# Kernel tuning notes

Measured on AMD Instinct MI355X. Metric: run time of the kernel, lower is better.

## Reference

```python
import jax, jax.numpy as jnp
import numpy as np

N = 50000
E = 300000
NEG_SLOPE = 0.2
EPS = 1e-16


def setup_inputs() -> dict:
    key = jax.random.key(0)
    ks = jax.random.split(key, 12)
    x = jax.random.normal(ks[0], (N, 27), dtype=jnp.float32)
    edge_index = jax.random.randint(ks[1], (2, E), 0, N, dtype=jnp.int64)
    # layer 1: in=27 -> heads1=4, dim=64
    W1 = jax.random.normal(ks[2], (27, 4 * 64), dtype=jnp.float32) * 0.1
    a_src1 = jax.random.normal(ks[3], (4, 64), dtype=jnp.float32) * 0.1
    a_dst1 = jax.random.normal(ks[4], (4, 64), dtype=jnp.float32) * 0.1
    b1 = jnp.zeros((4 * 64,), dtype=jnp.float32)
    # layer 2: in=256 -> heads2=2, dim=64
    W2 = jax.random.normal(ks[5], (256, 2 * 64), dtype=jnp.float32) * 0.05
    a_src2 = jax.random.normal(ks[6], (2, 64), dtype=jnp.float32) * 0.1
    a_dst2 = jax.random.normal(ks[7], (2, 64), dtype=jnp.float32) * 0.1
    b2 = jnp.zeros((2 * 64,), dtype=jnp.float32)
    # final linear: 128 -> 1
    Wfc = jax.random.normal(ks[8], (128, 1), dtype=jnp.float32) * 0.05
    bfc = jnp.zeros((1,), dtype=jnp.float32)
    return {"x": x, "edge_index": edge_index, "W1": W1, "a_src1": a_src1,
            "a_dst1": a_dst1, "b1": b1, "W2": W2, "a_src2": a_src2,
            "a_dst2": a_dst2, "b2": b2, "Wfc": Wfc, "bfc": bfc}


def gat_layer(x, src, dst, W, a_src, a_dst, b, heads, dim):
    # h: [N, H, D]
    h = (x @ W).reshape(N, heads, dim)
    # per-node attention half-scores: [N, H]
    s_src = jnp.einsum('nhd,hd->nh', h, a_src)
    s_dst = jnp.einsum('nhd,hd->nh', h, a_dst)
    # per-edge logits (gather) + leaky relu: [E', H]
    logits = jax.nn.leaky_relu(s_src[src] + s_dst[dst], negative_slope=NEG_SLOPE)
    # segment softmax over incoming edges at each destination node
    m = jax.ops.segment_max(logits, dst, num_segments=N)  # [N, H]
    m = jnp.where(jnp.isfinite(m), m, 0.0)
    e = jnp.exp(logits - m[dst])
    z = jax.ops.segment_sum(e, dst, num_segments=N)  # [N, H]
    alpha = e / (z[dst] + EPS)
    # weighted scatter-aggregate of source features
    out = jax.ops.segment_sum(h[src] * alpha[:, :, None], dst, num_segments=N)
    return out.reshape(N, heads * dim) + b


def reference(x, edge_index, W1, a_src1, a_dst1, b1, W2, a_src2, a_dst2, b2, Wfc, bfc):
    # add self-loops (PyG GATConv default add_self_loops=True)
    loops = jnp.arange(N, dtype=edge_index.dtype)
    src = jnp.concatenate([edge_index[0], loops])
    dst = jnp.concatenate([edge_index[1], loops])
    h = gat_layer(x, src, dst, W1, a_src1, a_dst1, b1, heads=4, dim=64)
    h = jax.nn.elu(h)
    h = gat_layer(h, src, dst, W2, a_src2, a_dst2, b2, heads=2, dim=64)
    h = jax.nn.elu(h)
    out = h @ Wfc + bfc
    return jax.nn.sigmoid(out)
```

## Files before the change

### kernel.cpp

```cpp
#include <hip/hip_runtime.h>
#include <math.h>

#define N_NODES 50000
#define N_PAD   50016
#define E_EDGES 300000
#define E_TOT   350000
#define NEG 0.2f
#define EPS 1e-16f
#define CAP 32
#define PLANE (N_PAD * 32)

typedef __attribute__((ext_vector_type(8))) short bf16x8;
typedef __attribute__((ext_vector_type(4))) float f32x4;

__device__ __forceinline__ float leaky(float x) { return x > 0.f ? x : NEG * x; }
__device__ __forceinline__ short f2bf(float v) {
    unsigned u = __float_as_uint(v);
    u += 0x7fffu + ((u >> 16) & 1u);
    return (short)(u >> 16);
}
__device__ __forceinline__ float bflo(unsigned u) { return __uint_as_float(u << 16); }
__device__ __forceinline__ float bfhi(unsigned u) { return __uint_as_float(u & 0xffff0000u); }
__device__ __forceinline__ unsigned bfpack(short a, short b) {
    return (unsigned)(unsigned short)a | ((unsigned)(unsigned short)b << 16);
}

__global__ __launch_bounds__(256) void k_scatter_s1(const int* __restrict__ ei,
        int* __restrict__ cnt, int* __restrict__ eidx,
        const float* __restrict__ x,
        const float* __restrict__ W1, const float* __restrict__ as1,
        const float* __restrict__ ad1, const float* __restrict__ W2,
        float* __restrict__ s1, short* __restrict__ xb,
        short* __restrict__ W1b, short* __restrict__ W2bT) {
    __shared__ float wsvL[216];
    int t = blockIdx.x * 256 + threadIdx.x;
    if (threadIdx.x < 216) {
        int k = threadIdx.x >> 3, j = threadIdx.x & 7;
        const float* av = (j < 4) ? (as1 + j * 64) : (ad1 + (j - 4) * 64);
        const float* wr = W1 + k * 256 + ((j & 3) * 64);
        float s = 0.f;
        #pragma unroll
        for (int d = 0; d < 64; ++d) s += wr[d] * av[d];
        wsvL[threadIdx.x] = s;
    }
    if (t < E_TOT) {
        int s = (t < E_EDGES) ? ei[t] : (t - E_EDGES);
        int d = (t < E_EDGES) ? ei[E_EDGES + t] : (t - E_EDGES);
        int pos = atomicAdd(&cnt[d], 1);
        if (pos < CAP) eidx[d * CAP + pos] = s;
    }
    if (t < 32768) {
        int col = t >> 8, k = t & 255;
        W2bT[t] = f2bf(W2[k * 128 + col]);
    }
    if (t < 8192) {
        int h = t >> 11, col = (t >> 5) & 63, k = t & 31;
        W1b[t] = f2bf(k < 27 ? W1[k * 256 + h * 64 + col] : 0.f);
    }
    __syncthreads();
    if (t < N_NODES * 8) {
        int n = t >> 3, j = t & 7;
        float s = 0.f;
        #pragma unroll
        for (int k = 0; k < 27; ++k) s += x[n * 27 + k] * wsvL[k * 8 + j];
        s1[t] = s;
        int c0 = j * 4;
        short p0 = f2bf(c0 + 0 < 27 ? x[n * 27 + c0 + 0] : 0.f);
        short p1 = f2bf(c0 + 1 < 27 ? x[n * 27 + c0 + 1] : 0.f);
        short p2 = f2bf(c0 + 2 < 27 ? x[n * 27 + c0 + 2] : 0.f);
        short p3 = f2bf(c0 + 3 < 27 ? x[n * 27 + c0 + 3] : 0.f);
        uint2 wv;
        wv.x = bfpack(p0, p1);
        wv.y = bfpack(p2, p3);
        *(uint2*)(xb + n * 32 + c0) = wv;
    }
}

__global__ __launch_bounds__(256) void k_gather1(const int* __restrict__ cnt,
        const int* __restrict__ eidx, const short* __restrict__ xb,
        const float* __restrict__ s1, short* __restrict__ xagg) {
    int g = threadIdx.x >> 4;
    int q = threadIdx.x & 15;
    int n = blockIdx.x * 16 + g;
    int c2 = 2 * q;
    if (n >= N_NODES) {
        if (n < N_PAD) {
            *(unsigned*)(xagg + 0 * PLANE + n * 32 + c2) = 0u;
            *(unsigned*)(xagg + 1 * PLANE + n * 32 + c2) = 0u;
            *(unsigned*)(xagg + 2 * PLANE + n * 32 + c2) = 0u;
            *(unsigned*)(xagg + 3 * PLANE + n * 32 + c2) = 0u;
        }
        return;
    }
    int beg = n * CAP;
    int espec = eidx[beg + q];
    int deg = min(cnt[n], CAP);
    int myi = (q < deg) ? espec : n;
    float4 sdv = *(const float4*)(s1 + n * 8 + 4);
    float a0 = 0.f, a1 = 0.f, a2 = 0.f, a3 = 0.f;
    float b0 = 0.f, b1v = 0.f, b2v = 0.f, b3 = 0.f;
    float z0 = 0.f, z1 = 0.f, z2 = 0.f, z3 = 0.f;
    float4 svq = *(const float4*)(s1 + myi * 8);
    float me0 = __expf(leaky(svq.x + sdv.x));
    float me1 = __expf(leaky(svq.y + sdv.y));
    float me2 = __expf(leaky(svq.z + sdv.z));
    float me3 = __expf(leaky(svq.w + sdv.w));
    int degw = deg;
    degw = max(degw, __shfl_xor(degw, 16));
    degw = max(degw, __shfl_xor(degw, 32));
    if (degw <= 16) {
        int lw = deg - 1;
        for (int i = 0; i < degw; i += 4) {
            bool m0 = i < deg, m1 = (i + 1) < deg;
            bool m2 = (i + 2) < deg, m3 = (i + 3) < deg;
            int j0 = m0 ? i : lw;
            int j1 = m1 ? i + 1 : lw;
            int j2 = m2 ? i + 2 : lw;
            int j3 = m3 ? i + 3 : lw;
            float g0 = m0 ? 1.f : 0.f, g1 = m1 ? 1.f : 0.f;
            float g2 = m2 ? 1.f : 0.f, g3 = m3 ? 1.f : 0.f;
            int s0 = __shfl(myi, j0, 16);
            int s1i = __shfl(myi, j1, 16);
            int s2i = __shfl(myi, j2, 16);
            int s3 = __shfl(myi, j3, 16);
            float e00 = g0 * __shfl(me0, j0, 16);
            float e01 = g0 * __shfl(me1, j0, 16);
            float e02 = g0 * __shfl(me2, j0, 16);
            float e03 = g0 * __shfl(me3, j0, 16);
            float e10 = g1 * __shfl(me0, j1, 16);
            float e11 = g1 * __shfl(me1, j1, 16);
            float e12 = g1 * __shfl(me2, j1, 16);
            float e13 = g1 * __shfl(me3, j1, 16);
            float e20 = g2 * __shfl(me0, j2, 16);
            float e21 = g2 * __shfl(me1, j2, 16);
            float e22 = g2 * __shfl(me2, j2, 16);
            float e23 = g2 * __shfl(me3, j2, 16);
            float e30 = g3 * __shfl(me0, j3, 16);
            float e31 = g3 * __shfl(me1, j3, 16);
            float e32 = g3 * __shfl(me2, j3, 16);
            float e33 = g3 * __shfl(me3, j3, 16);
            unsigned xv0 = *(const unsigned*)(xb + s0 * 32 + 2 * q);
            unsigned xv1 = *(const unsigned*)(xb + s1i * 32 + 2 * q);
            unsigned xv2 = *(const unsigned*)(xb + s2i * 32 + 2 * q);
            unsigned xv3 = *(const unsigned*)(xb + s3 * 32 + 2 * q);
            float xa0 = bflo(xv0), xc0 = bfhi(xv0);
            float xa1 = bflo(xv1), xc1 = bfhi(xv1);
            float xa2 = bflo(xv2), xc2 = bfhi(xv2);
            float xa3 = bflo(xv3), xc3 = bfhi(xv3);
            z0 += e00 + e10 + e20 + e30;
            z1 += e01 + e11 + e21 + e31;
            z2 += e02 + e12 + e22 + e32;
            z3 += e03 + e13 + e23 + e33;
            a0 += e00 * xa0 + e10 * xa1 + e20 * xa2 + e30 * xa3;
            a1 += e01 * xa0 + e11 * xa1 + e21 * xa2 + e31 * xa3;
            a2 += e02 * xa0 + e12 * xa1 + e22 * xa2 + e32 * xa3;
            a3 += e03 * xa0 + e13 * xa1 + e23 * xa2 + e33 * xa3;
            b0  += e00 * xc0 + e10 * xc1 + e20 * xc2 + e30 * xc3;
            b1v += e01 * xc0 + e11 * xc1 + e21 * xc2 + e31 * xc3;
            b2v += e02 * xc0 + e12 * xc1 + e22 * xc2 + e32 * xc3;
            b3  += e03 * xc0 + e13 * xc1 + e23 * xc2 + e33 * xc3;
        }
    } else {
        int last = beg + deg - 1;
        for (int i = 0; i < deg; i += 4) {
            bool m1 = (i + 1) < deg, m2 = (i + 2) < deg, m3 = (i + 3) < deg;
            int p0 = beg + i;
            int p1 = m1 ? p0 + 1 : last;
            int p2 = m2 ? p0 + 2 : last;
            int p3 = m3 ? p0 + 3 : last;
            int s0 = eidx[p0];
            int s1i = eidx[p1];
            int s2i = eidx[p2];
            int s3 = eidx[p3];
            float4 sv0 = *(const float4*)(s1 + s0 * 8);
            float4 sv1 = *(const float4*)(s1 + s1i * 8);
            float4 sv2 = *(const float4*)(s1 + s2i * 8);
            float4 sv3 = *(const float4*)(s1 + s3 * 8);
            unsigned xv0 = *(const unsigned*)(xb + s0 * 32 + 2 * q);
            unsigned xv1 = *(const unsigned*)(xb + s1i * 32 + 2 * q);
            unsigned xv2 = *(const unsigned*)(xb + s2i * 32 + 2 * q);
            unsigned xv3 = *(const unsigned*)(xb + s3 * 32 + 2 * q);
            float xa0 = bflo(xv0), xc0 = bfhi(xv0);
            float xa1 = bflo(xv1), xc1 = bfhi(xv1);
            float xa2 = bflo(xv2), xc2 = bfhi(xv2);
            float xa3 = bflo(xv3), xc3 = bfhi(xv3);
            float g1 = m1 ? 1.f : 0.f, g2 = m2 ? 1.f : 0.f, g3 = m3 ? 1.f : 0.f;
            float e00 = __expf(leaky(sv0.x + sdv.x));
            float e01 = __expf(leaky(sv0.y + sdv.y));
            float e02 = __expf(leaky(sv0.z + sdv.z));
            float e03 = __expf(leaky(sv0.w + sdv.w));
            float e10 = g1 * __expf(leaky(sv1.x + sdv.x));
            float e11 = g1 * __expf(leaky(sv1.y + sdv.y));
            float e12 = g1 * __expf(leaky(sv1.z + sdv.z));
            float e13 = g1 * __expf(leaky(sv1.w + sdv.w));
            float e20 = g2 * __expf(leaky(sv2.x + sdv.x));
            float e21 = g2 * __expf(leaky(sv2.y + sdv.y));
            float e22 = g2 * __expf(leaky(sv2.z + sdv.z));
            float e23 = g2 * __expf(leaky(sv2.w + sdv.w));
            float e30 = g3 * __expf(leaky(sv3.x + sdv.x));
            float e31 = g3 * __expf(leaky(sv3.y + sdv.y));
            float e32 = g3 * __expf(leaky(sv3.z + sdv.z));
            float e33 = g3 * __expf(leaky(sv3.w + sdv.w));
            z0 += e00 + e10 + e20 + e30;
            z1 += e01 + e11 + e21 + e31;
            z2 += e02 + e12 + e22 + e32;
            z3 += e03 + e13 + e23 + e33;
            a0 += e00 * xa0 + e10 * xa1 + e20 * xa2 + e30 * xa3;
            a1 += e01 * xa0 + e11 * xa1 + e21 * xa2 + e31 * xa3;
            a2 += e02 * xa0 + e12 * xa1 + e22 * xa2 + e32 * xa3;
            a3 += e03 * xa0 + e13 * xa1 + e23 * xa2 + e33 * xa3;
            b0  += e00 * xc0 + e10 * xc1 + e20 * xc2 + e30 * xc3;
            b1v += e01 * xc0 + e11 * xc1 + e21 * xc2 + e31 * xc3;
            b2v += e02 * xc0 + e12 * xc1 + e22 * xc2 + e32 * xc3;
            b3  += e03 * xc0 + e13 * xc1 + e23 * xc2 + e33 * xc3;
        }
    }
    float i0 = 1.f / (z0 + EPS), i1 = 1.f / (z1 + EPS);
    float i2 = 1.f / (z2 + EPS), i3 = 1.f / (z3 + EPS);
    *(unsigned*)(xagg + 0 * PLANE + n * 32 + c2) = bfpack(f2bf(a0 * i0), f2bf(b0 * i0));
    *(unsigned*)(xagg + 1 * PLANE + n * 32 + c2) = bfpack(f2bf(a1 * i1), f2bf(b1v * i1));
    *(unsigned*)(xagg + 2 * PLANE + n * 32 + c2) = bfpack(f2bf(a2 * i2), f2bf(b2v * i2));
    *(unsigned*)(xagg + 3 * PLANE + n * 32 + c2) = bfpack(f2bf(a3 * i3), f2bf(b3 * i3));
}

__global__ __launch_bounds__(256) void k_dense(const short* __restrict__ xagg,
        const short* __restrict__ W1b, const short* __restrict__ W2bT,
        const float* __restrict__ b1, const float* __restrict__ as2,
        const float* __restrict__ ad2, short* __restrict__ h2b,
        float* __restrict__ s2) {
    __shared__ short O[32 * 264];
    __shared__ float P[4][2][32];
    int w = threadIdx.x >> 6, l = threadIdx.x & 63;
    int lane16 = l & 15, quad = l >> 4;
    int n0 = blockIdx.x * 32;
    f32x4 z4 = {0.f, 0.f, 0.f, 0.f};

    {
        bf16x8 am0 = *(const bf16x8*)&xagg[w * PLANE + (n0 + lane16) * 32 + quad * 8];
        bf16x8 am1 = *(const bf16x8*)&xagg[w * PLANE + (n0 + 16 + lane16) * 32 + quad * 8];
        f32x4 c0[4], c1[4];
        #pragma unroll
        for (int nt = 0; nt < 4; ++nt) {
            bf16x8 b = *(const bf16x8*)&W1b[w * 2048 + (nt * 16 + lane16) * 32 + quad * 8];
            c0[nt] = __builtin_amdgcn_mfma_f32_16x16x32_bf16(am0, b, z4, 0, 0, 0);
            c1[nt] = __builtin_amdgcn_mfma_f32_16x16x32_bf16(am1, b, z4, 0, 0, 0);
        }
        #pragma unroll
        for (int nt = 0; nt < 4; ++nt) {
            int col = w * 64 + nt * 16 + lane16;
            float bb = b1[col];
            #pragma unroll
            for (int r2 = 0; r2 < 4; ++r2) {
                float v = c0[nt][r2] + bb;
                v = v > 0.f ? v : __expf(v) - 1.f;
                O[(quad * 4 + r2) * 264 + col] = f2bf(v);
                float u = c1[nt][r2] + bb;
                u = u > 0.f ? u : __expf(u) - 1.f;
                O[(16 + quad * 4 + r2) * 264 + col] = f2bf(u);
            }
        }
    }
    __syncthreads();

    f32x4 acc[2][2];
    acc[0][0] = z4; acc[0][1] = z4; acc[1][0] = z4; acc[1][1] = z4;
    for (int k0 = 0; k0 < 256; k0 += 32) {
        bf16x8 a0 = *(const bf16x8*)&O[lane16 * 264 + k0 + quad * 8];
        bf16x8 a1 = *(const bf16x8*)&O[(16 + lane16) * 264 + k0 + quad * 8];
        #pragma unroll
        for (int j = 0; j < 2; ++j) {
            int ct = 2 * w + j;
            bf16x8 b2 = *(const bf16x8*)&W2bT[(ct * 16 + lane16) * 256 + k0 + quad * 8];
            acc[0][j] = __builtin_amdgcn_mfma_f32_16x16x32_bf16(a0, b2, acc[0][j], 0, 0, 0);
            acc[1][j] = __builtin_amdgcn_mfma_f32_16x16x32_bf16(a1, b2, acc[1][j], 0, 0, 0);
        }
    }
    float ps[2][4] = {{0.f,0.f,0.f,0.f},{0.f,0.f,0.f,0.f}};
    float pd[2][4] = {{0.f,0.f,0.f,0.f},{0.f,0.f,0.f,0.f}};
    #pragma unroll
    for (int j = 0; j < 2; ++j) {
        int col = (2 * w + j) * 16 + lane16;
        float a_s = as2[col], a_d = ad2[col];
        #pragma unroll
        for (int m = 0; m < 2; ++m) {
            #pragma unroll
            for (int r2 = 0; r2 < 4; ++r2) {
                ps[m][r2] += acc[m][j][r2] * a_s;
                pd[m][r2] += acc[m][j][r2] * a_d;
                int row = n0 + m * 16 + quad * 4 + r2;
                if (row < N_NODES) h2b[row * 128 + col] = f2bf(acc[m][j][r2]);
            }
        }
    }
    #pragma unroll
    for (int off = 1; off <= 8; off <<= 1)
        #pragma unroll
        for (int m = 0; m < 2; ++m)
            #pragma unroll
            for (int r2 = 0; r2 < 4; ++r2) {
                ps[m][r2] += __shfl_xor(ps[m][r2], off);
                pd[m][r2] += __shfl_xor(pd[m][r2], off);
            }
    if (lane16 == 0) {
        #pragma unroll
        for (int m = 0; m < 2; ++m)
            #pragma unroll
            for (int r2 = 0; r2 < 4; ++r2) {
                P[w][0][m * 16 + quad * 4 + r2] = ps[m][r2];
                P[w][1][m * 16 + quad * 4 + r2] = pd[m][r2];
            }
    }
    __syncthreads();
    if (threadIdx.x < 64) {
        int m = threadIdx.x & 31, hd = threadIdx.x >> 5;
        int row = n0 + m;
        if (row < N_NODES) {
            s2[row * 4 + hd]     = P[2 * hd][0][m] + P[2 * hd + 1][0][m];
            s2[row * 4 + 2 + hd] = P[2 * hd][1][m] + P[2 * hd + 1][1][m];
        }
    }
}

__global__ __launch_bounds__(256) void k_agg2_csr(const int* __restrict__ cnt,
        const int* __restrict__ eidx, const float* __restrict__ s2,
        const short* __restrict__ h2b, const float* __restrict__ b2,
        const float* __restrict__ Wfc, const float* __restrict__ bfc,
        float* __restrict__ out) {
    int g = threadIdx.x >> 4;
    int q = threadIdx.x & 15;
    int n = blockIdx.x * 16 + g;
    int beg = n * CAP;
    int espec = eidx[beg + q];
    int deg = min(cnt[n], CAP);
    int myi = (q < deg) ? espec : n;
    int h = q >> 3;
    float2 sdv = *(const float2*)(s2 + n * 4 + 2);
    float4 accA = make_float4(0.f, 0.f, 0.f, 0.f);
    float4 accB = make_float4(0.f, 0.f, 0.f, 0.f);
    float z = 0.f;
    float2 svq = *(const float2*)(s2 + myi * 4);
    float mea = __expf(leaky(svq.x + sdv.x));
    float meb = __expf(leaky(svq.y + sdv.y));
    int degw = deg;
    degw = max(degw, __shfl_xor(degw, 16));
    degw = max(degw, __shfl_xor(degw, 32));
    if (degw <= 16) {
        int lw = deg - 1;
        for (int i = 0; i < degw; i += 4) {
            bool m0 = i < deg, m1 = (i + 1) < deg;
            bool m2 = (i + 2) < deg, m3 = (i + 3) < deg;
            int j0 = m0 ? i : lw;
            int j1 = m1 ? i + 1 : lw;
            int j2 = m2 ? i + 2 : lw;
            int j3 = m3 ? i + 3 : lw;
            int a0 = __shfl(myi, j0, 16);
            int a1 = __shfl(myi, j1, 16);
            int a2 = __shfl(myi, j2, 16);
            int a3 = __shfl(myi, j3, 16);
            float ea0 = __shfl(mea, j0, 16), eb0 = __shfl(meb, j0, 16);
            float ea1 = __shfl(mea, j1, 16), eb1 = __shfl(meb, j1, 16);
            float ea2 = __shfl(mea, j2, 16), eb2 = __shfl(meb, j2, 16);
            float ea3 = __shfl(mea, j3, 16), eb3 = __shfl(meb, j3, 16);
            float e0 = (m0 ? 1.f : 0.f) * (h ? eb0 : ea0);
            float e1 = (m1 ? 1.f : 0.f) * (h ? eb1 : ea1);
            float e2 = (m2 ? 1.f : 0.f) * (h ? eb2 : ea2);
            float e3 = (m3 ? 1.f : 0.f) * (h ? eb3 : ea3);
            uint4 v0 = *(const uint4*)(h2b + a0 * 128 + q * 8);
            uint4 v1 = *(const uint4*)(h2b + a1 * 128 + q * 8);
            uint4 v2 = *(const uint4*)(h2b + a2 * 128 + q * 8);
            uint4 v3 = *(const uint4*)(h2b + a3 * 128 + q * 8);
            z += e0 + e1 + e2 + e3;
            accA.x += e0 * bflo(v0.x) + e1 * bflo(v1.x) + e2 * bflo(v2.x) + e3 * bflo(v3.x);
            accA.y += e0 * bfhi(v0.x) + e1 * bfhi(v1.x) + e2 * bfhi(v2.x) + e3 * bfhi(v3.x);
            accA.z += e0 * bflo(v0.y) + e1 * bflo(v1.y) + e2 * bflo(v2.y) + e3 * bflo(v3.y);
            accA.w += e0 * bfhi(v0.y) + e1 * bfhi(v1.y) + e2 * bfhi(v2.y) + e3 * bfhi(v3.y);
            accB.x += e0 * bflo(v0.z) + e1 * bflo(v1.z) + e2 * bflo(v2.z) + e3 * bflo(v3.z);
            accB.y += e0 * bfhi(v0.z) + e1 * bfhi(v1.z) + e2 * bfhi(v2.z) + e3 * bfhi(v3.z);
            accB.z += e0 * bflo(v0.w) + e1 * bflo(v1.w) + e2 * bflo(v2.w) + e3 * bflo(v3.w);
            accB.w += e0 * bfhi(v0.w) + e1 * bfhi(v1.w) + e2 * bfhi(v2.w) + e3 * bfhi(v3.w);
        }
    } else {
        float sd = h ? sdv.y : sdv.x;
        int i = 0;
        for (; i + 4 <= deg; i += 4) {
            int a0 = eidx[beg + i], a1 = eidx[beg + i + 1];
            int a2 = eidx[beg + i + 2], a3 = eidx[beg + i + 3];
            float e0 = __expf(leaky(s2[a0 * 4 + h] + sd));
            float e1 = __expf(leaky(s2[a1 * 4 + h] + sd));
            float e2 = __expf(leaky(s2[a2 * 4 + h] + sd));
            float e3 = __expf(leaky(s2[a3 * 4 + h] + sd));
            uint4 v0 = *(const uint4*)(h2b + a0 * 128 + q * 8);
            uint4 v1 = *(const uint4*)(h2b + a1 * 128 + q * 8);
            uint4 v2 = *(const uint4*)(h2b + a2 * 128 + q * 8);
            uint4 v3 = *(const uint4*)(h2b + a3 * 128 + q * 8);
            z += e0 + e1 + e2 + e3;
            accA.x += e0 * bflo(v0.x) + e1 * bflo(v1.x) + e2 * bflo(v2.x) + e3 * bflo(v3.x);
            accA.y += e0 * bfhi(v0.x) + e1 * bfhi(v1.x) + e2 * bfhi(v2.x) + e3 * bfhi(v3.x);
            accA.z += e0 * bflo(v0.y) + e1 * bflo(v1.y) + e2 * bflo(v2.y) + e3 * bflo(v3.y);
            accA.w += e0 * bfhi(v0.y) + e1 * bfhi(v1.y) + e2 * bfhi(v2.y) + e3 * bfhi(v3.y);
            accB.x += e0 * bflo(v0.z) + e1 * bflo(v1.z) + e2 * bflo(v2.z) + e3 * bflo(v3.z);
            accB.y += e0 * bfhi(v0.z) + e1 * bfhi(v1.z) + e2 * bfhi(v2.z) + e3 * bfhi(v3.z);
            accB.z += e0 * bflo(v0.w) + e1 * bflo(v1.w) + e2 * bflo(v2.w) + e3 * bflo(v3.w);
            accB.w += e0 * bfhi(v0.w) + e1 * bfhi(v1.w) + e2 * bfhi(v2.w) + e3 * bfhi(v3.w);
        }
        for (; i < deg; ++i) {
            int a0 = eidx[beg + i];
            float e0 = __expf(leaky(s2[a0 * 4 + h] + sd));
            uint4 v0 = *(const uint4*)(h2b + a0 * 128 + q * 8);
            z += e0;
            accA.x += e0 * bflo(v0.x); accA.y += e0 * bfhi(v0.x);
            accA.z += e0 * bflo(v0.y); accA.w += e0 * bfhi(v0.y);
            accB.x += e0 * bflo(v0.z); accB.y += e0 * bfhi(v0.z);
            accB.z += e0 * bflo(v0.w); accB.w += e0 * bfhi(v0.w);
        }
    }
    float inv = 1.f / (z + EPS);
    int c0 = q * 8;
    float p = 0.f;
    float va[8] = {accA.x, accA.y, accA.z, accA.w, accB.x, accB.y, accB.z, accB.w};
    #pragma unroll
    for (int j = 0; j < 8; ++j) {
        float v = va[j] * inv + b2[c0 + j];
        v = v > 0.f ? v : __expf(v) - 1.f;
        p += v * Wfc[c0 + j];
    }
    #pragma unroll
    for (int off = 1; off <= 8; off <<= 1) p += __shfl_xor(p, off);
    if (q == 0) out[n] = 1.f / (1.f + __expf(-(p + bfc[0])));
}

extern "C" void kernel_launch(void* const* d_in, const int* in_sizes, int n_in,
                              void* d_out, int out_size, void* d_ws, size_t ws_size,
                              hipStream_t stream) {
    const float* x   = (const float*)d_in[0];
    const int*   ei  = (const int*)d_in[1];
    const float* W1  = (const float*)d_in[2];
    const float* as1 = (const float*)d_in[3];
    const float* ad1 = (const float*)d_in[4];
    const float* b1  = (const float*)d_in[5];
    const float* W2  = (const float*)d_in[6];
    const float* as2 = (const float*)d_in[7];
    const float* ad2 = (const float*)d_in[8];
    const float* b2  = (const float*)d_in[9];
    const float* Wfc = (const float*)d_in[10];
    const float* bfc = (const float*)d_in[11];
    float* out = (float*)d_out;

    float* f = (float*)d_ws;
    short* h2b   = (short*)f;
    float* s1    = f + 3200000;
    float* s2    = f + 3600000;
    int*   cnt   = (int*)(f + 3810000);
    int*   eidx  = (int*)(f + 3870000);
    short* W1b   = (short*)(f + 5500000);
    short* W2bT  = (short*)(f + 5510000);
    short* xb    = (short*)(f + 5530000);
    short* xagg  = (short*)(f + 6400000);

    hipMemsetAsync(cnt, 0, N_NODES * sizeof(int), stream);

    k_scatter_s1<<<1563, 256, 0, stream>>>(ei, cnt, eidx, x, W1, as1, ad1, W2,
                                           s1, xb, W1b, W2bT);

    k_gather1<<<3126, 256, 0, stream>>>(cnt, eidx, xb, s1, xagg);

    k_dense<<<1563, 256, 0, stream>>>(xagg, W1b, W2bT, b1, as2, ad2, h2b, s2);

    k_agg2_csr<<<3125, 256, 0, stream>>>(cnt, eidx, s2, h2b, b2, Wfc, bfc, out);
}
```

Baseline: 167.7 us.

## Widen layer-2 aggregation to 32 lanes per node, batch gathers, stage x in LDS

The layer-2 aggregation kernel now gives each node 32 lanes with 4 channels each instead of 16 lanes with 8 channels, and the launch grid doubles to match. Both gather kernels replace the 4-wide masked loop with fixed 8-edge batches whose loads are issued together before accumulation, aiming for more memory-level parallelism on the random gathers. The first kernel stages each block's x rows in shared memory so they are read from global memory once rather than repeatedly per thread. The trade-off is padded work for low-degree nodes, since at least 8 slots are always processed, plus the added reduction step and thread count.

```diff
diff --git a/kernel.cpp b/kernel.cpp
--- a/kernel.cpp
+++ b/kernel.cpp
@@ -33,15 +33,23 @@
         float* __restrict__ s1, short* __restrict__ xb,
         short* __restrict__ W1b, short* __restrict__ W2bT) {
     __shared__ float wsvL[216];
-    int t = blockIdx.x * 256 + threadIdx.x;
-    if (threadIdx.x < 216) {
-        int k = threadIdx.x >> 3, j = threadIdx.x & 7;
+    __shared__ float xL[32 * 27];
+    int tid = threadIdx.x;
+    int t = blockIdx.x * 256 + tid;
+    int nb = blockIdx.x * 32;
+    #pragma unroll
+    for (int i = tid; i < 864; i += 256) {
+        int gi = nb * 27 + i;
+        xL[i] = (gi < N_NODES * 27) ? x[gi] : 0.f;
+    }
+    if (tid < 216) {
+        int k = tid >> 3, j = tid & 7;
         const float* av = (j < 4) ? (as1 + j * 64) : (ad1 + (j - 4) * 64);
         const float* wr = W1 + k * 256 + ((j & 3) * 64);
         float s = 0.f;
         #pragma unroll
         for (int d = 0; d < 64; ++d) s += wr[d] * av[d];
-        wsvL[threadIdx.x] = s;
+        wsvL[tid] = s;
     }
     if (t < E_TOT) {
         int s = (t < E_EDGES) ? ei[t] : (t - E_EDGES);
@@ -59,20 +67,22 @@
     }
     __syncthreads();
     if (t < N_NODES * 8) {
-        int n = t >> 3, j = t & 7;
+        int ln = tid >> 3, j = tid & 7;
+        int n = nb + ln;
         float s = 0.f;
         #pragma unroll
-        for (int k = 0; k < 27; ++k) s += x[n * 27 + k] * wsvL[k * 8 + j];
+        for (int k = 0; k < 27; ++k) s += xL[ln * 27 + k] * wsvL[k * 8 + j];
         s1[t] = s;
         int c0 = j * 4;
-        short p0 = f2bf(c0 + 0 < 27 ? x[n * 27 + c0 + 0] : 0.f);
-        short p1 = f2bf(c0 + 1 < 27 ? x[n * 27 + c0 + 1] : 0.f);
-        short p2 = f2bf(c0 + 2 < 27 ? x[n * 27 + c0 + 2] : 0.f);
-        short p3 = f2bf(c0 + 3 < 27 ? x[n * 27 + c0 + 3] : 0.f);
+        short p0 = f2bf(c0 + 0 < 27 ? xL[ln * 27 + c0 + 0] : 0.f);
+        short p1 = f2bf(c0 + 1 < 27 ? xL[ln * 27 + c0 + 1] : 0.f);
+        short p2 = f2bf(c0 + 2 < 27 ? xL[ln * 27 + c0 + 2] : 0.f);
+        short p3 = f2bf(c0 + 3 < 27 ? xL[ln * 27 + c0 + 3] : 0.f);
         uint2 wv;
         wv.x = bfpack(p0, p1);
         wv.y = bfpack(p2, p3);
         *(uint2*)(xb + n * 32 + c0) = wv;
+        (void)n;
     }
 }
 
@@ -109,56 +119,45 @@
     degw = max(degw, __shfl_xor(degw, 16));
     degw = max(degw, __shfl_xor(degw, 32));
     if (degw <= 16) {
-        int lw = deg - 1;
-        for (int i = 0; i < degw; i += 4) {
-            bool m0 = i < deg, m1 = (i + 1) < deg;
-            bool m2 = (i + 2) < deg, m3 = (i + 3) < deg;
-            int j0 = m0 ? i : lw;
-            int j1 = m1 ? i + 1 : lw;
-            int j2 = m2 ? i + 2 : lw;
-            int j3 = m3 ? i + 3 : lw;
-            float g0 = m0 ? 1.f : 0.f, g1 = m1 ? 1.f : 0.f;
-            float g2 = m2 ? 1.f : 0.f, g3 = m3 ? 1.f : 0.f;
-            int s0 = __shfl(myi, j0, 16);
-            int s1i = __shfl(myi, j1, 16);
-            int s2i = __shfl(myi, j2, 16);
-            int s3 = __shfl(myi, j3, 16);
-            float e00 = g0 * __shfl(me0, j0, 16);
-            float e01 = g0 * __shfl(me1, j0, 16);
-            float e02 = g0 * __shfl(me2, j0, 16);
-            float e03 = g0 * __shfl(me3, j0, 16);
-            float e10 = g1 * __shfl(me0, j1, 16);
-            float e11 = g1 * __shfl(me1, j1, 16);
-            float e12 = g1 * __shfl(me2, j1, 16);
-            float e13 = g1 * __shfl(me3, j1, 16);
-            float e20 = g2 * __shfl(me0, j2, 16);
-            float e21 = g2 * __shfl(me1, j2, 16);
-            float e22 = g2 * __shfl(me2, j2, 16);
-            float e23 = g2 * __shfl(me3, j2, 16);
-            float e30 = g3 * __shfl(me0, j3, 16);
-            float e31 = g3 * __shfl(me1, j3, 16);
-            float e32 = g3 * __shfl(me2, j3, 16);
-            float e33 = g3 * __shfl(me3, j3, 16);
-            unsigned xv0 = *(const unsigned*)(xb + s0 * 32 + 2 * q);
-            unsigned xv1 = *(const unsigned*)(xb + s1i * 32 + 2 * q);
-            unsigned xv2 = *(const unsigned*)(xb + s2i * 32 + 2 * q);
-            unsigned xv3 = *(const unsigned*)(xb + s3 * 32 + 2 * q);
-            float xa0 = bflo(xv0), xc0 = bfhi(xv0);
-            float xa1 = bflo(xv1), xc1 = bfhi(xv1);
-            float xa2 = bflo(xv2), xc2 = bfhi(xv2);
-            float xa3 = bflo(xv3), xc3 = bfhi(xv3);
-            z0 += e00 + e10 + e20 + e30;
-            z1 += e01 + e11 + e21 + e31;
-            z2 += e02 + e12 + e22 + e32;
-            z3 += e03 + e13 + e23 + e33;
-            a0 += e00 * xa0 + e10 * xa1 + e20 * xa2 + e30 * xa3;
-            a1 += e01 * xa0 + e11 * xa1 + e21 * xa2 + e31 * xa3;
-            a2 += e02 * xa0 + e12 * xa1 + e22 * xa2 + e32 * xa3;
-            a3 += e03 * xa0 + e13 * xa1 + e23 * xa2 + e33 * xa3;
-            b0  += e00 * xc0 + e10 * xc1 + e20 * xc2 + e30 * xc3;
-            b1v += e01 * xc0 + e11 * xc1 + e21 * xc2 + e31 * xc3;
-            b2v += e02 * xc0 + e12 * xc1 + e22 * xc2 + e32 * xc3;
-            b3  += e03 * xc0 + e13 * xc1 + e23 * xc2 + e33 * xc3;
+        {
+            unsigned xv[8];
+            #pragma unroll
+            for (int j = 0; j < 8; ++j) {
+                int sj = __shfl(myi, j, 16);
+                xv[j] = *(const unsigned*)(xb + sj * 32 + c2);
+            }
+            #pragma unroll
+            for (int j = 0; j < 8; ++j) {
+                float gj = (j < deg) ? 1.f : 0.f;
+                float e0 = gj * __shfl(me0, j, 16);
+                float e1 = gj * __shfl(me1, j, 16);
+                float e2 = gj * __shfl(me2, j, 16);
+                float e3 = gj * __shfl(me3, j, 16);
+                float xa = bflo(xv[j]), xc = bfhi(xv[j]);
+                z0 += e0; z1 += e1; z2 += e2; z3 += e3;
+                a0 += e0 * xa; a1 += e1 * xa; a2 += e2 * xa; a3 += e3 * xa;
+                b0 += e0 * xc; b1v += e1 * xc; b2v += e2 * xc; b3 += e3 * xc;
+            }
+        }
+        if (degw > 8) {
+            unsigned xv[8];
+            #pragma unroll
+            for (int j = 0; j < 8; ++j) {
+                int sj = __shfl(myi, 8 + j, 16);
+                xv[j] = *(const unsigned*)(xb + sj * 32 + c2);
+            }
+            #pragma unroll
+            for (int j = 0; j < 8; ++j) {
+                float gj = (8 + j < deg) ? 1.f : 0.f;
+                float e0 = gj * __shfl(me0, 8 + j, 16);
+                float e1 = gj * __shfl(me1, 8 + j, 16);
+                float e2 = gj * __shfl(me2, 8 + j, 16);
+                float e3 = gj * __shfl(me3, 8 + j, 16);
+                float xa = bflo(xv[j]), xc = bfhi(xv[j]);
+                z0 += e0; z1 += e1; z2 += e2; z3 += e3;
+                a0 += e0 * xa; a1 += e1 * xa; a2 += e2 * xa; a3 += e3 * xa;
+                b0 += e0 * xc; b1v += e1 * xc; b2v += e2 * xc; b3 += e3 * xc;
+            }
         }
     } else {
         int last = beg + deg - 1;
@@ -176,10 +175,10 @@
             float4 sv1 = *(const float4*)(s1 + s1i * 8);
             float4 sv2 = *(const float4*)(s1 + s2i * 8);
             float4 sv3 = *(const float4*)(s1 + s3 * 8);
-            unsigned xv0 = *(const unsigned*)(xb + s0 * 32 + 2 * q);
-            unsigned xv1 = *(const unsigned*)(xb + s1i * 32 + 2 * q);
-            unsigned xv2 = *(const unsigned*)(xb + s2i * 32 + 2 * q);
-            unsigned xv3 = *(const unsigned*)(xb + s3 * 32 + 2 * q);
+            unsigned xv0 = *(const unsigned*)(xb + s0 * 32 + c2);
+            unsigned xv1 = *(const unsigned*)(xb + s1i * 32 + c2);
+            unsigned xv2 = *(const unsigned*)(xb + s2i * 32 + c2);
+            unsigned xv3 = *(const unsigned*)(xb + s3 * 32 + c2);
             float xa0 = bflo(xv0), xc0 = bfhi(xv0);
             float xa1 = bflo(xv1), xc1 = bfhi(xv1);
             float xa2 = bflo(xv2), xc2 = bfhi(xv2);
@@ -326,58 +325,54 @@
         const short* __restrict__ h2b, const float* __restrict__ b2,
         const float* __restrict__ Wfc, const float* __restrict__ bfc,
         float* __restrict__ out) {
-    int g = threadIdx.x >> 4;
-    int q = threadIdx.x & 15;
-    int n = blockIdx.x * 16 + g;
+    int g = threadIdx.x >> 5;
+    int q = threadIdx.x & 31;
+    int n = blockIdx.x * 8 + g;
     int beg = n * CAP;
-    int espec = eidx[beg + q];
+    int q16 = q & 15;
+    int espec = eidx[beg + q16];
     int deg = min(cnt[n], CAP);
-    int myi = (q < deg) ? espec : n;
-    int h = q >> 3;
+    int myi = (q16 < deg) ? espec : n;
+    int h = q >> 4;
     float2 sdv = *(const float2*)(s2 + n * 4 + 2);
-    float4 accA = make_float4(0.f, 0.f, 0.f, 0.f);
-    float4 accB = make_float4(0.f, 0.f, 0.f, 0.f);
+    float ac0 = 0.f, ac1 = 0.f, ac2 = 0.f, ac3 = 0.f;
     float z = 0.f;
     float2 svq = *(const float2*)(s2 + myi * 4);
     float mea = __expf(leaky(svq.x + sdv.x));
     float meb = __expf(leaky(svq.y + sdv.y));
-    int degw = deg;
-    degw = max(degw, __shfl_xor(degw, 16));
-    degw = max(degw, __shfl_xor(degw, 32));
+    int degw = max(deg, __shfl_xor(deg, 32));
     if (degw <= 16) {
-        int lw = deg - 1;
-        for (int i = 0; i < degw; i += 4) {
-            bool m0 = i < deg, m1 = (i + 1) < deg;
-            bool m2 = (i + 2) < deg, m3 = (i + 3) < deg;
-            int j0 = m0 ? i : lw;
-            int j1 = m1 ? i + 1 : lw;
-            int j2 = m2 ? i + 2 : lw;
-            int j3 = m3 ? i + 3 : lw;
-            int a0 = __shfl(myi, j0, 16);
-            int a1 = __shfl(myi, j1, 16);
-            int a2 = __shfl(myi, j2, 16);
-            int a3 = __shfl(myi, j3, 16);
-            float ea0 = __shfl(mea, j0, 16), eb0 = __shfl(meb, j0, 16);
-            float ea1 = __shfl(mea, j1, 16), eb1 = __shfl(meb, j1, 16);
-            float ea2 = __shfl(mea, j2, 16), eb2 = __shfl(meb, j2, 16);
-            float ea3 = __shfl(mea, j3, 16), eb3 = __shfl(meb, j3, 16);
-            float e0 = (m0 ? 1.f : 0.f) * (h ? eb0 : ea0);
-            float e1 = (m1 ? 1.f : 0.f) * (h ? eb1 : ea1);
-            float e2 = (m2 ? 1.f : 0.f) * (h ? eb2 : ea2);
-            float e3 = (m3 ? 1.f : 0.f) * (h ? eb3 : ea3);
-            uint4 v0 = *(const uint4*)(h2b + a0 * 128 + q * 8);
-            uint4 v1 = *(const uint4*)(h2b + a1 * 128 + q * 8);
-            uint4 v2 = *(const uint4*)(h2b + a2 * 128 + q * 8);
-            uint4 v3 = *(const uint4*)(h2b + a3 * 128 + q * 8);
-            z += e0 + e1 + e2 + e3;
-            accA.x += e0 * bflo(v0.x) + e1 * bflo(v1.x) + e2 * bflo(v2.x) + e3 * bflo(v3.x);
-            accA.y += e0 * bfhi(v0.x) + e1 * bfhi(v1.x) + e2 * bfhi(v2.x) + e3 * bfhi(v3.x);
-            accA.z += e0 * bflo(v0.y) + e1 * bflo(v1.y) + e2 * bflo(v2.y) + e3 * bflo(v3.y);
-            accA.w += e0 * bfhi(v0.y) + e1 * bfhi(v1.y) + e2 * bfhi(v2.y) + e3 * bfhi(v3.y);
-            accB.x += e0 * bflo(v0.z) + e1 * bflo(v1.z) + e2 * bflo(v2.z) + e3 * bflo(v3.z);
-            accB.y += e0 * bfhi(v0.z) + e1 * bfhi(v1.z) + e2 * bfhi(v2.z) + e3 * bfhi(v3.z);
-            accB.z += e0 * bflo(v0.w) + e1 * bflo(v1.w) + e2 * bflo(v2.w) + e3 * bflo(v3.w);
-            accB.w += e0 * bfhi(v0.w) + e1 * bfhi(v1.w) + e2 * bfhi(v2.w) + e3 * bfhi(v3.w);
+        {
+            uint2 v[8];
+            #pragma unroll
+            for (int j = 0; j < 8; ++j) {
+                int aj = __shfl(myi, j, 32);
+                v[j] = *(const uint2*)(h2b + aj * 128 + q * 4);
+            }
+            #pragma unroll
+            for (int j = 0; j < 8; ++j) {
+                float ea = __shfl(mea, j, 32), eb = __shfl(meb, j, 32);
+                float e = ((j < deg) ? 1.f : 0.f) * (h ? eb : ea);
+                z += e;
+                ac0 += e * bflo(v[j].x); ac1 += e * bfhi(v[j].x);
+                ac2 += e * bflo(v[j].y); ac3 += e * bfhi(v[j].y);
+            }
+        }
+        if (degw > 8) {
+            uint2 v[8];
+            #pragma unroll
+            for (int j = 0; j < 8; ++j) {
+                int aj = __shfl(myi, 8 + j, 32);
+                v[j] = *(const uint2*)(h2b + aj * 128 + q * 4);
+            }
+            #pragma unroll
+            for (int j = 0; j < 8; ++j) {
+                float ea = __shfl(mea, 8 + j, 32), eb = __shfl(meb, 8 + j, 32);
+                float e = ((8 + j < deg) ? 1.f : 0.f) * (h ? eb : ea);
+                z += e;
+                ac0 += e * bflo(v[j].x); ac1 += e * bfhi(v[j].x);
+                ac2 += e * bflo(v[j].y); ac3 += e * bfhi(v[j].y);
+            }
         }
     } else {
         float sd = h ? sdv.y : sdv.x;
@@ -389,43 +384,37 @@
             float e1 = __expf(leaky(s2[a1 * 4 + h] + sd));
             float e2 = __expf(leaky(s2[a2 * 4 + h] + sd));
             float e3 = __expf(leaky(s2[a3 * 4 + h] + sd));
-            uint4 v0 = *(const uint4*)(h2b + a0 * 128 + q * 8);
-            uint4 v1 = *(const uint4*)(h2b + a1 * 128 + q * 8);
-            uint4 v2 = *(const uint4*)(h2b + a2 * 128 + q * 8);
-            uint4 v3 = *(const uint4*)(h2b + a3 * 128 + q * 8);
+            uint2 v0 = *(const uint2*)(h2b + a0 * 128 + q * 4);
+            uint2 v1 = *(const uint2*)(h2b + a1 * 128 + q * 4);
+            uint2 v2 = *(const uint2*)(h2b + a2 * 128 + q * 4);
+            uint2 v3 = *(const uint2*)(h2b + a3 * 128 + q * 4);
             z += e0 + e1 + e2 + e3;
-            accA.x += e0 * bflo(v0.x) + e1 * bflo(v1.x) + e2 * bflo(v2.x) + e3 * bflo(v3.x);
-            accA.y += e0 * bfhi(v0.x) + e1 * bfhi(v1.x) + e2 * bfhi(v2.x) + e3 * bfhi(v3.x);
-            accA.z += e0 * bflo(v0.y) + e1 * bflo(v1.y) + e2 * bflo(v2.y) + e3 * bflo(v3.y);
-            accA.w += e0 * bfhi(v0.y) + e1 * bfhi(v1.y) + e2 * bfhi(v2.y) + e3 * bfhi(v3.y);
-            accB.x += e0 * bflo(v0.z) + e1 * bflo(v1.z) + e2 * bflo(v2.z) + e3 * bflo(v3.z);
-            accB.y += e0 * bfhi(v0.z) + e1 * bfhi(v1.z) + e2 * bfhi(v2.z) + e3 * bfhi(v3.z);
-            accB.z += e0 * bflo(v0.w) + e1 * bflo(v1.w) + e2 * bflo(v2.w) + e3 * bflo(v3.w);
-            accB.w += e0 * bfhi(v0.w) + e1 * bfhi(v1.w) + e2 * bfhi(v2.w) + e3 * bfhi(v3.w);
+            ac0 += e0 * bflo(v0.x) + e1 * bflo(v1.x) + e2 * bflo(v2.x) + e3 * bflo(v3.x);
+            ac1 += e0 * bfhi(v0.x) + e1 * bfhi(v1.x) + e2 * bfhi(v2.x) + e3 * bfhi(v3.x);
+            ac2 += e0 * bflo(v0.y) + e1 * bflo(v1.y) + e2 * bflo(v2.y) + e3 * bflo(v3.y);
+            ac3 += e0 * bfhi(v0.y) + e1 * bfhi(v1.y) + e2 * bfhi(v2.y) + e3 * bfhi(v3.y);
         }
         for (; i < deg; ++i) {
             int a0 = eidx[beg + i];
             float e0 = __expf(leaky(s2[a0 * 4 + h] + sd));
-            uint4 v0 = *(const uint4*)(h2b + a0 * 128 + q * 8);
+            uint2 v0 = *(const uint2*)(h2b + a0 * 128 + q * 4);
             z += e0;
-            accA.x += e0 * bflo(v0.x); accA.y += e0 * bfhi(v0.x);
-            accA.z += e0 * bflo(v0.y); accA.w += e0 * bfhi(v0.y);
-            accB.x += e0 * bflo(v0.z); accB.y += e0 * bfhi(v0.z);
-            accB.z += e0 * bflo(v0.w); accB.w += e0 * bfhi(v0.w);
+            ac0 += e0 * bflo(v0.x); ac1 += e0 * bfhi(v0.x);
+            ac2 += e0 * bflo(v0.y); ac3 += e0 * bfhi(v0.y);
         }
     }
     float inv = 1.f / (z + EPS);
-    int c0 = q * 8;
+    int c0 = q * 4;
     float p = 0.f;
-    float va[8] = {accA.x, accA.y, accA.z, accA.w, accB.x, accB.y, accB.z, accB.w};
+    float va[4] = {ac0, ac1, ac2, ac3};
     #pragma unroll
-    for (int j = 0; j < 8; ++j) {
+    for (int j = 0; j < 4; ++j) {
         float v = va[j] * inv + b2[c0 + j];
         v = v > 0.f ? v : __expf(v) - 1.f;
         p += v * Wfc[c0 + j];
     }
     #pragma unroll
-    for (int off = 1; off <= 8; off <<= 1) p += __shfl_xor(p, off);
+    for (int off = 1; off <= 16; off <<= 1) p += __shfl_xor(p, off, 32);
     if (q == 0) out[n] = 1.f / (1.f + __expf(-(p + bfc[0])));
 }
 
@@ -466,5 +455,5 @@
 
     k_dense<<<1563, 256, 0, stream>>>(xagg, W1b, W2bT, b1, as2, ad2, h2b, s2);
 
-    k_agg2_csr<<<3125, 256, 0, stream>>>(cnt, eidx, s2, h2b, b2, Wfc, bfc, out);
-}
+    k_agg2_csr<<<6250, 256, 0, stream>>>(cnt, eidx, s2, h2b, b2, Wfc, bfc, out);
+}
```

New measurement: 171.0 us. No clear change (+1.9%).
